# Kernel optimization log

Hardware: AMD Instinct MI355X
Metric: run time of the kernel (lower is better)

## Reference

```python
import jax, jax.numpy as jnp
import numpy as np

N = 20000; E = 320000; IN = 512; H = 4; C = 128; HC = H * C; SD = 2; SE = 128
NEG = 0.01      # nn.LeakyReLU default slope (post-norm activations)
ATT_NEG = 0.2   # GATv2 attention LeakyReLU slope


def _gatv2(x, wl, bl, wr, br, att, bias, src, dst, concat):
    # PyG GATv2Conv (eval mode, add_self_loops already applied to src/dst)
    n = x.shape[0]
    xl = (x @ wl.T + bl).reshape(n, H, C)   # source-side projection
    xr = (x @ wr.T + br).reshape(n, H, C)   # target-side projection
    e = jax.nn.leaky_relu(xl[src] + xr[dst], ATT_NEG)        # [Etot, H, C]
    logits = jnp.einsum('ehc,hc->eh', e, att)                # [Etot, H]
    m = jax.ops.segment_max(logits, dst, num_segments=n)     # segment softmax over dst
    ez = jnp.exp(logits - m[dst])
    denom = jax.ops.segment_sum(ez, dst, num_segments=n)
    alpha = ez / denom[dst]
    out = jax.ops.segment_sum(xl[src] * alpha[:, :, None], dst, num_segments=n)  # [n, H, C]
    out = out.reshape(n, HC) if concat else out.mean(axis=1)
    return out + bias, alpha


def _bn(x, g, b):
    # BatchNorm1d, training-mode batch statistics (biased variance), eps=1e-5
    mu = x.mean(0)
    v = x.var(0)
    return g * (x - mu) * jax.lax.rsqrt(v + 1e-5) + b


def setup_inputs() -> dict:
    key = jax.random.key(0)
    ks = jax.random.split(key, 20)
    p = lambda i, shape: jax.random.normal(ks[i], shape, jnp.float32) * 0.05
    return dict(
        x=jax.random.normal(ks[0], (N, IN), jnp.float32),
        edge_index=jax.random.randint(ks[1], (2, E), 0, N),
        spatial_coords=jax.random.uniform(ks[2], (N, SD), dtype=jnp.float32),
        w1_l=p(3, (HC, IN)), b1_l=jnp.zeros((HC,)), w1_r=p(4, (HC, IN)), b1_r=jnp.zeros((HC,)),
        att1=p(5, (H, C)), bias1=jnp.zeros((HC,)), bn1_g=jnp.ones((HC,)), bn1_b=jnp.zeros((HC,)),
        w2_l=p(6, (HC, HC)), b2_l=jnp.zeros((HC,)), w2_r=p(7, (HC, HC)), b2_r=jnp.zeros((HC,)),
        att2=p(8, (H, C)), bias2=jnp.zeros((HC,)), bn2_g=jnp.ones((HC,)), bn2_b=jnp.zeros((HC,)),
        w3_l=p(9, (HC, HC)), b3_l=jnp.zeros((HC,)), w3_r=p(10, (HC, HC)), b3_r=jnp.zeros((HC,)),
        att3=p(11, (H, C)), bias3=jnp.zeros((C,)), bn3_g=jnp.ones((C,)), bn3_b=jnp.zeros((C,)),
        sp_w1=p(12, (SE, SD)), sp_b1=jnp.zeros((SE,)),
        sp_w2=p(13, (C, SE)), sp_b2=jnp.zeros((C,)),
        mha_in_w=p(14, (3 * SE, SE)), mha_in_b=jnp.zeros((3 * SE,)),
        mha_out_w=p(15, (SE, SE)), mha_out_b=jnp.zeros((SE,)),
        gate_w=p(16, (1, 2 * C)), gate_b=jnp.zeros((1,)),
    )


def reference(x, edge_index, spatial_coords,
              w1_l, b1_l, w1_r, b1_r, att1, bias1, bn1_g, bn1_b,
              w2_l, b2_l, w2_r, b2_r, att2, bias2, bn2_g, bn2_b,
              w3_l, b3_l, w3_r, b3_r, att3, bias3, bn3_g, bn3_b,
              sp_w1, sp_b1, sp_w2, sp_b2,
              mha_in_w, mha_in_b, mha_out_w, mha_out_b,
              gate_w, gate_b):
    loop = jnp.arange(N)
    src = jnp.concatenate([edge_index[0], loop])  # add self loops (PyG default)
    dst = jnp.concatenate([edge_index[1], loop])

    h1, a1 = _gatv2(x, w1_l, b1_l, w1_r, b1_r, att1, bias1, src, dst, True)
    h1 = jax.nn.leaky_relu(_bn(h1, bn1_g, bn1_b), NEG)
    h2, a2 = _gatv2(h1, w2_l, b2_l, w2_r, b2_r, att2, bias2, src, dst, True)
    h2 = jax.nn.leaky_relu(_bn(h2, bn2_g, bn2_b), NEG)
    z, a3 = _gatv2(h2, w3_l, b3_l, w3_r, b3_r, att3, bias3, src, dst, False)
    z = jax.nn.leaky_relu(_bn(z, bn3_g, bn3_b), NEG)

    # spatial embedding MLP (Linear -> LeakyReLU -> Linear -> LeakyReLU)
    emb = jax.nn.leaky_relu(spatial_coords @ sp_w1.T + sp_b1, NEG)
    emb = jax.nn.leaky_relu(emb @ sp_w2.T + sp_b2, NEG)
    # MultiheadAttention over a length-1 sequence: softmax over a single key is 1,
    # so output = W_o (W_v e + b_v) + b_o
    wv = mha_in_w[2 * SE:]
    bv = mha_in_b[2 * SE:]
    sp = (emb @ wv.T + bv) @ mha_out_w.T + mha_out_b  # [N, C]

    gate = jax.nn.softmax(jnp.concatenate([z, sp], axis=-1) @ gate_w.T + gate_b, axis=-1)  # [N,1] (all ones: size-1 softmax, faithful to source)
    z = gate * z + (1.0 - gate) * sp
    return z, a1, a2, a3, gate
```

## Files before the change

### kernel.cpp

```cpp
#include <hip/hip_runtime.h>
#include <math.h>

#define NN 20000
#define EE 320000
#define ETOT 340000
#define MPAD 20096
#define DEGCAP 256

typedef __attribute__((ext_vector_type(8))) short short8;
typedef __attribute__((ext_vector_type(4))) float f32x4;

__device__ __forceinline__ float lrelu(float x, float s) { return fmaxf(x, s * x); }
__device__ __forceinline__ float bf2f(ushort u) {
    union { uint i; float f; } c;
    c.i = ((uint)u) << 16;
    return c.f;
}
__device__ __forceinline__ ushort f2bf(float f) {
    uint u = __float_as_uint(f);
    uint r = (u + 0x7FFFu + ((u >> 16) & 1u)) >> 16;
    return (ushort)r;
}
__device__ __forceinline__ void gload16(const ushort* g, ushort* l) {
    __builtin_amdgcn_global_load_lds((const __attribute__((address_space(1))) void*)g,
                                     (__attribute__((address_space(3))) void*)l, 16, 0, 0);
}

__global__ void k_count(const int* __restrict__ ei, int* __restrict__ counts) {
    int i = blockIdx.x * blockDim.x + threadIdx.x;
    if (i >= ETOT) return;
    int d = (i < EE) ? ei[EE + i] : (i - EE);
    atomicAdd(&counts[d], 1);
}

__global__ __launch_bounds__(1024) void k_scan(const int* __restrict__ counts, int* __restrict__ rstart) {
    __shared__ int sm[1024];
    int t = threadIdx.x;
    const int CH = 20;
    int base = t * CH;
    int loc[CH];
    int s = 0;
#pragma unroll
    for (int j = 0; j < CH; ++j) {
        int idx = base + j;
        int v = (idx < NN) ? counts[idx] : 0;
        loc[j] = s;
        s += v;
    }
    sm[t] = s;
    __syncthreads();
    for (int o = 1; o < 1024; o <<= 1) {
        int v = (t >= o) ? sm[t - o] : 0;
        __syncthreads();
        if (t >= o) sm[t] += v;
        __syncthreads();
    }
    int off = sm[t] - s;
#pragma unroll
    for (int j = 0; j < CH; ++j) {
        int idx = base + j;
        if (idx < NN) rstart[idx] = off + loc[j];
    }
    if (t == 1023) rstart[NN] = sm[1023];
}

__global__ void k_scatter(const int* __restrict__ ei, const int* __restrict__ rstart,
                          int* __restrict__ cursor, int* __restrict__ csr) {
    int i = blockIdx.x * blockDim.x + threadIdx.x;
    if (i >= ETOT) return;
    int d = (i < EE) ? ei[EE + i] : (i - EE);
    int pos = atomicAdd(&cursor[d], 1);
    csr[rstart[d] + pos] = i;
}

__global__ void k_cast(const float* __restrict__ in, ushort* __restrict__ out, int n) {
    int i = (blockIdx.x * blockDim.x + threadIdx.x) * 4;
    if (i >= n) return;
    float4 v = *(const float4*)(in + i);
    uint2 pk;
    pk.x = (uint)f2bf(v.x) | ((uint)f2bf(v.y) << 16);
    pk.y = (uint)f2bf(v.z) | ((uint)f2bf(v.w) << 16);
    *(uint2*)(out + i) = pk;
}

__global__ void k_castw(const float* __restrict__ w0, const float* __restrict__ w1, const float* __restrict__ w2,
                        const float* __restrict__ w3, const float* __restrict__ w4, const float* __restrict__ w5,
                        ushort* __restrict__ out) {
    int i = blockIdx.x * blockDim.x + threadIdx.x;
    if (i >= 6 * 65536) return;
    int which = i >> 16;
    int off = (i & 65535) << 2;
    const float* src = which == 0 ? w0 : which == 1 ? w1 : which == 2 ? w2 : which == 3 ? w3 : which == 4 ? w4 : w5;
    float4 v = *(const float4*)(src + off);
    uint2 pk;
    pk.x = (uint)f2bf(v.x) | ((uint)f2bf(v.y) << 16);
    pk.y = (uint)f2bf(v.z) | ((uint)f2bf(v.w) << 16);
    *(uint2*)(out + which * 262144 + off) = pk;
}

__global__ __launch_bounds__(256) void k_gemm(const ushort* __restrict__ A, const ushort* __restrict__ W,
                                              const float* __restrict__ bias, ushort* __restrict__ C, int M) {
    __shared__ ushort As[4][128][8];
    __shared__ ushort Bs[4][128][8];
    int tid = threadIdx.x;
    int wid = tid >> 6, lane = tid & 63;
    int wm = wid >> 1, wn = wid & 1;
    int bm = blockIdx.x * 128, bn = blockIdx.y * 128;
    int lrow = lane & 15, lslot = lane >> 4;
    int f0 = tid, f1 = tid + 256;
    int r0 = f0 & 127, ks0 = f0 >> 7;
    int r1 = f1 & 127, ks1 = f1 >> 7;
    const ushort* ga0 = A + (size_t)(bm + r0) * 512 + ks0 * 8;
    const ushort* ga1 = A + (size_t)(bm + r1) * 512 + ks1 * 8;
    const ushort* gb0 = W + (size_t)(bn + r0) * 512 + ks0 * 8;
    const ushort* gb1 = W + (size_t)(bn + r1) * 512 + ks1 * 8;
    ushort* lA = &As[0][0][0];
    ushort* lB = &Bs[0][0][0];
    ushort* lA0 = lA + (size_t)(wid * 64) * 8;
    ushort* lA1 = lA + (size_t)(256 + wid * 64) * 8;
    ushort* lB0 = lB + (size_t)(wid * 64) * 8;
    ushort* lB1 = lB + (size_t)(256 + wid * 64) * 8;
    f32x4 acc[4][4] = {};
    for (int k0 = 0; k0 < 512; k0 += 32) {
        gload16(ga0 + k0, lA0);
        gload16(ga1 + k0, lA1);
        gload16(gb0 + k0, lB0);
        gload16(gb1 + k0, lB1);
        __syncthreads();
        short8 af[4], bfr[4];
#pragma unroll
        for (int i = 0; i < 4; ++i) af[i] = *(const short8*)&As[lslot][wm * 64 + i * 16 + lrow][0];
#pragma unroll
        for (int j = 0; j < 4; ++j) bfr[j] = *(const short8*)&Bs[lslot][wn * 64 + j * 16 + lrow][0];
#pragma unroll
        for (int i = 0; i < 4; ++i)
#pragma unroll
            for (int j = 0; j < 4; ++j)
                acc[i][j] = __builtin_amdgcn_mfma_f32_16x16x32_bf16(af[i], bfr[j], acc[i][j], 0, 0, 0);
        __syncthreads();
    }
#pragma unroll
    for (int i = 0; i < 4; ++i) {
#pragma unroll
        for (int j = 0; j < 4; ++j) {
            int gcol = bn + wn * 64 + j * 16 + lrow;
            float bv = bias[gcol];
            int growb = bm + wm * 64 + i * 16 + lslot * 4;
#pragma unroll
            for (int reg = 0; reg < 4; ++reg) {
                int grow = growb + reg;
                if (grow < M) C[(size_t)grow * 512 + gcol] = f2bf(acc[i][j][reg] + bv);
            }
        }
    }
}

__global__ __launch_bounds__(256) void k_fused(const ushort* __restrict__ xl, const ushort* __restrict__ xr,
                                               const float* __restrict__ att, const int* __restrict__ ei,
                                               const int* __restrict__ rstart, const int* __restrict__ csr,
                                               const float* __restrict__ bias, float* __restrict__ alpha,
                                               float* __restrict__ dest, int meanHeads) {
    __shared__ float slg[4][DEGCAP][4];
    __shared__ int ssrc[4][DEGCAP];
    int w = threadIdx.x >> 6, lane = threadIdx.x & 63;
    int node = blockIdx.x * 4 + w;
    int s0 = rstart[node];
    int deg = rstart[node + 1] - s0;
    int hh = lane >> 4;
    short8 xrv = *(const short8*)(xr + (size_t)node * 512 + lane * 8);
    const float4* at = (const float4*)att + lane * 2;
    float4 a0 = at[0], a1 = at[1];
    float attv[8] = {a0.x, a0.y, a0.z, a0.w, a1.x, a1.y, a1.z, a1.w};
    float xrf[8];
#pragma unroll
    for (int j = 0; j < 8; ++j) xrf[j] = bf2f((ushort)xrv[j]);
    for (int i = lane; i < deg; i += 64) {
        int e = csr[s0 + i];
        ssrc[w][i < DEGCAP ? i : 0] = (e < EE) ? ei[e] : e - EE;
    }
    float m = -1e30f, denom = 0.f;
    float acc[8] = {};
    int scur = ssrc[w][0];
    short8 row = *(const short8*)(xl + (size_t)scur * 512 + lane * 8);
    for (int i = 0; i < deg; ++i) {
        short8 rown = row;
        if (i + 1 < deg) {
            int sn = ssrc[w][(i + 1) < DEGCAP ? (i + 1) : 0];
            rown = *(const short8*)(xl + (size_t)sn * 512 + lane * 8);
        }
        float rf[8];
#pragma unroll
        for (int j = 0; j < 8; ++j) rf[j] = bf2f((ushort)row[j]);
        float p = 0.f;
#pragma unroll
        for (int j = 0; j < 8; ++j) {
            float e = rf[j] + xrf[j];
            p = fmaf(fmaxf(e, 0.2f * e), attv[j], p);
        }
        p += __shfl_xor(p, 1);
        p += __shfl_xor(p, 2);
        p += __shfl_xor(p, 4);
        p += __shfl_xor(p, 8);
        if ((lane & 15) == 0 && i < DEGCAP) slg[w][i][hh] = p;
        float mn = fmaxf(m, p);
        float sc = __expf(m - mn);
        float wg = __expf(p - mn);
        denom = denom * sc + wg;
#pragma unroll
        for (int j = 0; j < 8; ++j) acc[j] = acc[j] * sc + wg * rf[j];
        m = mn;
        row = rown;
    }
    float rd = 1.f / denom;
    float m0 = __shfl(m, 0), m1 = __shfl(m, 16), m2 = __shfl(m, 32), m3 = __shfl(m, 48);
    float r0 = __shfl(rd, 0), r1 = __shfl(rd, 16), r2 = __shfl(rd, 32), r3 = __shfl(rd, 48);
    int nal = deg < DEGCAP ? deg : DEGCAP;
    for (int i = lane; i < nal; i += 64) {
        int e = csr[s0 + i];
        float4 l = *(const float4*)&slg[w][i][0];
        float4 av;
        av.x = __expf(l.x - m0) * r0;
        av.y = __expf(l.y - m1) * r1;
        av.z = __expf(l.z - m2) * r2;
        av.w = __expf(l.w - m3) * r3;
        *(float4*)(alpha + (size_t)e * 4) = av;
    }
#pragma unroll
    for (int j = 0; j < 8; ++j) acc[j] *= rd;
    if (!meanHeads) {
        int c = lane * 8;
        float4 o0, o1;
        o0.x = acc[0] + bias[c + 0]; o0.y = acc[1] + bias[c + 1];
        o0.z = acc[2] + bias[c + 2]; o0.w = acc[3] + bias[c + 3];
        o1.x = acc[4] + bias[c + 4]; o1.y = acc[5] + bias[c + 5];
        o1.z = acc[6] + bias[c + 6]; o1.w = acc[7] + bias[c + 7];
        float4* o = (float4*)(dest + (size_t)node * 512 + c);
        o[0] = o0;
        o[1] = o1;
    } else {
#pragma unroll
        for (int j = 0; j < 8; ++j) {
            acc[j] += __shfl_xor(acc[j], 16);
            acc[j] += __shfl_xor(acc[j], 32);
        }
        if (lane < 16) {
            int c = lane * 8;
#pragma unroll
            for (int j = 0; j < 8; ++j) dest[(size_t)node * 128 + c + j] = 0.25f * acc[j] + bias[c + j];
        }
    }
}

__global__ void k_bnstats(const float* __restrict__ X, float* __restrict__ s, float* __restrict__ s2, int ncols) {
    int col = threadIdx.x;
    float a = 0.f, q = 0.f;
    for (int r = blockIdx.x; r < NN; r += gridDim.x) {
        float v = X[(size_t)r * ncols + col];
        a += v;
        q += v * v;
    }
    atomicAdd(&s[col], a);
    atomicAdd(&s2[col], q);
}

__global__ void k_bnfin(const float* __restrict__ s, const float* __restrict__ s2, float* __restrict__ mu,
                        float* __restrict__ rs, int ncols) {
    int c = threadIdx.x;
    if (c < ncols) {
        float m = s[c] * (1.f / NN);
        float v = s2[c] * (1.f / NN) - m * m;
        mu[c] = m;
        rs[c] = rsqrtf(v + 1e-5f);
    }
}

__global__ void k_bnapply(const float* __restrict__ X, const float* __restrict__ g, const float* __restrict__ b,
                          const float* __restrict__ mu, const float* __restrict__ rs, float* __restrict__ Yf,
                          ushort* __restrict__ Yb, int mask4, int n4) {
    int i = blockIdx.x * blockDim.x + threadIdx.x;
    if (i >= n4) return;
    int c = (i & mask4) << 2;
    float4 x = ((const float4*)X)[i];
    float4 G = *(const float4*)(g + c);
    float4 B = *(const float4*)(b + c);
    float4 M = *(const float4*)(mu + c);
    float4 R = *(const float4*)(rs + c);
    float4 y;
    y.x = lrelu(G.x * (x.x - M.x) * R.x + B.x, 0.01f);
    y.y = lrelu(G.y * (x.y - M.y) * R.y + B.y, 0.01f);
    y.z = lrelu(G.z * (x.z - M.z) * R.z + B.z, 0.01f);
    y.w = lrelu(G.w * (x.w - M.w) * R.w + B.w, 0.01f);
    if (Yb) {
        uint2 pk;
        pk.x = (uint)f2bf(y.x) | ((uint)f2bf(y.y) << 16);
        pk.y = (uint)f2bf(y.z) | ((uint)f2bf(y.w) << 16);
        *(uint2*)(Yb + (size_t)i * 4) = pk;
    } else {
        ((float4*)Yf)[i] = y;
    }
}

__global__ void k_gate(float* __restrict__ g) {
    int i = blockIdx.x * blockDim.x + threadIdx.x;
    if (i < NN) g[i] = 1.0f;
}

extern "C" void kernel_launch(void* const* d_in, const int* in_sizes, int n_in,
                              void* d_out, int out_size, void* d_ws, size_t ws_size,
                              hipStream_t stream) {
    const float* x = (const float*)d_in[0];
    const int* ei = (const int*)d_in[1];
    const float* wl[3] = {(const float*)d_in[3], (const float*)d_in[11], (const float*)d_in[19]};
    const float* bl[3] = {(const float*)d_in[4], (const float*)d_in[12], (const float*)d_in[20]};
    const float* wr[3] = {(const float*)d_in[5], (const float*)d_in[13], (const float*)d_in[21]};
    const float* br[3] = {(const float*)d_in[6], (const float*)d_in[14], (const float*)d_in[22]};
    const float* att[3] = {(const float*)d_in[7], (const float*)d_in[15], (const float*)d_in[23]};
    const float* bias[3] = {(const float*)d_in[8], (const float*)d_in[16], (const float*)d_in[24]};
    const float* bng[3] = {(const float*)d_in[9], (const float*)d_in[17], (const float*)d_in[25]};
    const float* bnb[3] = {(const float*)d_in[10], (const float*)d_in[18], (const float*)d_in[26]};

    ushort* a_bf = (ushort*)d_ws;
    ushort* xl_bf = a_bf + (size_t)MPAD * 512;
    ushort* xr_bf = xl_bf + 10240000;
    ushort* wbuf = xr_bf + 10240000;
    float* fp = (float*)(wbuf + 6 * 262144);
    float* h = fp;
    float* zp = h + 10240000;
    float* bsum = zp + 2560000;
    float* bsq = bsum + 512;
    float* bmu = bsq + 512;
    float* brs = bmu + 512;
    int* counts = (int*)(brs + 512);
    int* cursor = counts + NN;
    int* rstart = cursor + NN;
    int* csr = rstart + (NN + 1);
    size_t need = (size_t)((char*)(csr + ETOT) - (char*)d_ws);
    if (ws_size < need) return;

    float* out = (float*)d_out;
    float* zout = out;
    float* aout[3] = {out + 2560000, out + 3920000, out + 5280000};
    float* gout = out + 6640000;

    hipMemsetAsync(counts, 0, 2 * NN * sizeof(int), stream);
    k_count<<<(ETOT + 255) / 256, 256, 0, stream>>>(ei, counts);
    k_scan<<<1, 1024, 0, stream>>>(counts, rstart);
    k_scatter<<<(ETOT + 255) / 256, 256, 0, stream>>>(ei, rstart, cursor, csr);

    hipMemsetAsync(a_bf + (size_t)NN * 512, 0, (size_t)(MPAD - NN) * 512 * sizeof(ushort), stream);
    k_cast<<<(NN * 512 / 4 + 255) / 256, 256, 0, stream>>>(x, a_bf, NN * 512);
    k_castw<<<(6 * 65536 + 255) / 256, 256, 0, stream>>>(wl[0], wr[0], wl[1], wr[1], wl[2], wr[2], wbuf);

    for (int l = 0; l < 3; ++l) {
        const ushort* wlb = wbuf + (size_t)(2 * l) * 262144;
        const ushort* wrb = wbuf + (size_t)(2 * l + 1) * 262144;
        dim3 gg(MPAD / 128, 4);
        k_gemm<<<gg, 256, 0, stream>>>(a_bf, wlb, bl[l], xl_bf, NN);
        k_gemm<<<gg, 256, 0, stream>>>(a_bf, wrb, br[l], xr_bf, NN);
        int ncols = (l == 2) ? 128 : 512;
        float* dest = (l == 2) ? zp : h;
        k_fused<<<NN / 4, 256, 0, stream>>>(xl_bf, xr_bf, att[l], ei, rstart, csr, bias[l], aout[l], dest,
                                            (l == 2) ? 1 : 0);
        hipMemsetAsync(bsum, 0, 1024 * sizeof(float), stream);
        k_bnstats<<<240, ncols, 0, stream>>>(dest, bsum, bsq, ncols);
        k_bnfin<<<1, ncols, 0, stream>>>(bsum, bsq, bmu, brs, ncols);
        int n4 = NN * ncols / 4;
        if (l < 2) {
            k_bnapply<<<(n4 + 255) / 256, 256, 0, stream>>>(dest, bng[l], bnb[l], bmu, brs, nullptr, a_bf,
                                                            ncols / 4 - 1, n4);
        } else {
            k_bnapply<<<(n4 + 255) / 256, 256, 0, stream>>>(dest, bng[l], bnb[l], bmu, brs, zout, nullptr,
                                                            ncols / 4 - 1, n4);
        }
    }
    k_gate<<<(NN + 255) / 256, 256, 0, stream>>>(gout);
}
```

Before: 732.8 us.

## Merge L/R GEMMs, store GAT outputs in bf16, branchy online softmax

Combines the source and target projection GEMMs into one launch with a swizzled tile order and row clamping, removing the padded-row memset. GAT layer outputs are written in bf16, and batchnorm stats/apply read bf16 pairs, cutting intermediate traffic. The online softmax update branches to avoid one exp per edge, and the per-node degree cap in shared memory is halved. This risks precision loss from bf16 intermediates and dropped alphas for nodes with very high degree.

```diff
diff --git a/kernel.cpp b/kernel.cpp
--- a/kernel.cpp
+++ b/kernel.cpp
@@ -4,8 +4,7 @@
 #define NN 20000
 #define EE 320000
 #define ETOT 340000
-#define MPAD 20096
-#define DEGCAP 256
+#define DEGCAP 128
 
 typedef __attribute__((ext_vector_type(8))) short short8;
 typedef __attribute__((ext_vector_type(4))) float f32x4;
@@ -98,20 +97,29 @@
     *(uint2*)(out + which * 262144 + off) = pk;
 }
 
-__global__ __launch_bounds__(256) void k_gemm(const ushort* __restrict__ A, const ushort* __restrict__ W,
-                                              const float* __restrict__ bias, ushort* __restrict__ C, int M) {
+__global__ __launch_bounds__(256) void k_gemm2(const ushort* __restrict__ A, const ushort* __restrict__ W,
+                                               const float* __restrict__ bl, const float* __restrict__ br,
+                                               ushort* __restrict__ XL, ushort* __restrict__ XR) {
     __shared__ ushort As[4][128][8];
     __shared__ ushort Bs[4][128][8];
     int tid = threadIdx.x;
     int wid = tid >> 6, lane = tid & 63;
     int wm = wid >> 1, wn = wid & 1;
-    int bm = blockIdx.x * 128, bn = blockIdx.y * 128;
+    int bid = blockIdx.x;
+    int L = (bid & 7) * 157 + (bid >> 3);
+    int mt = L >> 3, nt = L & 7;
+    int bm = mt * 128, bn = nt * 128;
+    const float* bias = (nt >= 4) ? br : bl;
+    ushort* C = (nt >= 4) ? XR : XL;
+    int cb = bn - ((nt >= 4) ? 512 : 0);
     int lrow = lane & 15, lslot = lane >> 4;
     int f0 = tid, f1 = tid + 256;
     int r0 = f0 & 127, ks0 = f0 >> 7;
     int r1 = f1 & 127, ks1 = f1 >> 7;
-    const ushort* ga0 = A + (size_t)(bm + r0) * 512 + ks0 * 8;
-    const ushort* ga1 = A + (size_t)(bm + r1) * 512 + ks1 * 8;
+    int ar0 = bm + r0; if (ar0 >= NN) ar0 = NN - 1;
+    int ar1 = bm + r1; if (ar1 >= NN) ar1 = NN - 1;
+    const ushort* ga0 = A + (size_t)ar0 * 512 + ks0 * 8;
+    const ushort* ga1 = A + (size_t)ar1 * 512 + ks1 * 8;
     const ushort* gb0 = W + (size_t)(bn + r0) * 512 + ks0 * 8;
     const ushort* gb1 = W + (size_t)(bn + r1) * 512 + ks1 * 8;
     ushort* lA = &As[0][0][0];
@@ -143,13 +151,13 @@
     for (int i = 0; i < 4; ++i) {
 #pragma unroll
         for (int j = 0; j < 4; ++j) {
-            int gcol = bn + wn * 64 + j * 16 + lrow;
+            int gcol = cb + wn * 64 + j * 16 + lrow;
             float bv = bias[gcol];
             int growb = bm + wm * 64 + i * 16 + lslot * 4;
 #pragma unroll
             for (int reg = 0; reg < 4; ++reg) {
                 int grow = growb + reg;
-                if (grow < M) C[(size_t)grow * 512 + gcol] = f2bf(acc[i][j][reg] + bv);
+                if (grow < NN) C[(size_t)grow * 512 + gcol] = f2bf(acc[i][j][reg] + bv);
             }
         }
     }
@@ -159,7 +167,7 @@
                                                const float* __restrict__ att, const int* __restrict__ ei,
                                                const int* __restrict__ rstart, const int* __restrict__ csr,
                                                const float* __restrict__ bias, float* __restrict__ alpha,
-                                               float* __restrict__ dest, int meanHeads) {
+                                               ushort* __restrict__ dest, int meanHeads) {
     __shared__ float slg[4][DEGCAP][4];
     __shared__ int ssrc[4][DEGCAP];
     int w = threadIdx.x >> 6, lane = threadIdx.x & 63;
@@ -202,13 +210,18 @@
         p += __shfl_xor(p, 4);
         p += __shfl_xor(p, 8);
         if ((lane & 15) == 0 && i < DEGCAP) slg[w][i][hh] = p;
-        float mn = fmaxf(m, p);
-        float sc = __expf(m - mn);
-        float wg = __expf(p - mn);
-        denom = denom * sc + wg;
-#pragma unroll
-        for (int j = 0; j < 8; ++j) acc[j] = acc[j] * sc + wg * rf[j];
-        m = mn;
+        if (p <= m) {
+            float wg = __expf(p - m);
+            denom += wg;
+#pragma unroll
+            for (int j = 0; j < 8; ++j) acc[j] = fmaf(wg, rf[j], acc[j]);
+        } else {
+            float sc = __expf(m - p);
+            denom = fmaf(denom, sc, 1.f);
+#pragma unroll
+            for (int j = 0; j < 8; ++j) acc[j] = fmaf(acc[j], sc, rf[j]);
+            m = p;
+        }
         row = rown;
     }
     float rd = 1.f / denom;
@@ -229,14 +242,10 @@
     for (int j = 0; j < 8; ++j) acc[j] *= rd;
     if (!meanHeads) {
         int c = lane * 8;
-        float4 o0, o1;
-        o0.x = acc[0] + bias[c + 0]; o0.y = acc[1] + bias[c + 1];
-        o0.z = acc[2] + bias[c + 2]; o0.w = acc[3] + bias[c + 3];
-        o1.x = acc[4] + bias[c + 4]; o1.y = acc[5] + bias[c + 5];
-        o1.z = acc[6] + bias[c + 6]; o1.w = acc[7] + bias[c + 7];
-        float4* o = (float4*)(dest + (size_t)node * 512 + c);
-        o[0] = o0;
-        o[1] = o1;
+        short8 o;
+#pragma unroll
+        for (int j = 0; j < 8; ++j) o[j] = (short)f2bf(acc[j] + bias[c + j]);
+        *(short8*)(dest + (size_t)node * 512 + c) = o;
     } else {
 #pragma unroll
         for (int j = 0; j < 8; ++j) {
@@ -245,22 +254,29 @@
         }
         if (lane < 16) {
             int c = lane * 8;
-#pragma unroll
-            for (int j = 0; j < 8; ++j) dest[(size_t)node * 128 + c + j] = 0.25f * acc[j] + bias[c + j];
-        }
-    }
-}
-
-__global__ void k_bnstats(const float* __restrict__ X, float* __restrict__ s, float* __restrict__ s2, int ncols) {
-    int col = threadIdx.x;
-    float a = 0.f, q = 0.f;
+            short8 o;
+#pragma unroll
+            for (int j = 0; j < 8; ++j) o[j] = (short)f2bf(0.25f * acc[j] + bias[c + j]);
+            *(short8*)(dest + (size_t)node * 128 + c) = o;
+        }
+    }
+}
+
+__global__ void k_bnstats(const ushort* __restrict__ X, float* __restrict__ s, float* __restrict__ s2, int npairs) {
+    int t = threadIdx.x;
+    if (t >= npairs) return;
+    float a0 = 0.f, a1 = 0.f, q0 = 0.f, q1 = 0.f;
     for (int r = blockIdx.x; r < NN; r += gridDim.x) {
-        float v = X[(size_t)r * ncols + col];
-        a += v;
-        q += v * v;
-    }
-    atomicAdd(&s[col], a);
-    atomicAdd(&s2[col], q);
+        uint p = ((const uint*)X)[r * npairs + t];
+        float v0 = bf2f((ushort)(p & 0xffffu));
+        float v1 = bf2f((ushort)(p >> 16));
+        a0 += v0; q0 += v0 * v0;
+        a1 += v1; q1 += v1 * v1;
+    }
+    atomicAdd(&s[2 * t], a0);
+    atomicAdd(&s[2 * t + 1], a1);
+    atomicAdd(&s2[2 * t], q0);
+    atomicAdd(&s2[2 * t + 1], q1);
 }
 
 __global__ void k_bnfin(const float* __restrict__ s, const float* __restrict__ s2, float* __restrict__ mu,
@@ -274,22 +290,24 @@
     }
 }
 
-__global__ void k_bnapply(const float* __restrict__ X, const float* __restrict__ g, const float* __restrict__ b,
+__global__ void k_bnapply(const ushort* __restrict__ X, const float* __restrict__ g, const float* __restrict__ b,
                           const float* __restrict__ mu, const float* __restrict__ rs, float* __restrict__ Yf,
                           ushort* __restrict__ Yb, int mask4, int n4) {
     int i = blockIdx.x * blockDim.x + threadIdx.x;
     if (i >= n4) return;
     int c = (i & mask4) << 2;
-    float4 x = ((const float4*)X)[i];
+    uint2 p = ((const uint2*)X)[i];
+    float x0 = bf2f((ushort)(p.x & 0xffffu)), x1 = bf2f((ushort)(p.x >> 16));
+    float x2 = bf2f((ushort)(p.y & 0xffffu)), x3 = bf2f((ushort)(p.y >> 16));
     float4 G = *(const float4*)(g + c);
     float4 B = *(const float4*)(b + c);
     float4 M = *(const float4*)(mu + c);
     float4 R = *(const float4*)(rs + c);
     float4 y;
-    y.x = lrelu(G.x * (x.x - M.x) * R.x + B.x, 0.01f);
-    y.y = lrelu(G.y * (x.y - M.y) * R.y + B.y, 0.01f);
-    y.z = lrelu(G.z * (x.z - M.z) * R.z + B.z, 0.01f);
-    y.w = lrelu(G.w * (x.w - M.w) * R.w + B.w, 0.01f);
+    y.x = lrelu(G.x * (x0 - M.x) * R.x + B.x, 0.01f);
+    y.y = lrelu(G.y * (x1 - M.y) * R.y + B.y, 0.01f);
+    y.z = lrelu(G.z * (x2 - M.z) * R.z + B.z, 0.01f);
+    y.w = lrelu(G.w * (x3 - M.w) * R.w + B.w, 0.01f);
     if (Yb) {
         uint2 pk;
         pk.x = (uint)f2bf(y.x) | ((uint)f2bf(y.y) << 16);
@@ -320,13 +338,12 @@
     const float* bnb[3] = {(const float*)d_in[10], (const float*)d_in[18], (const float*)d_in[26]};
 
     ushort* a_bf = (ushort*)d_ws;
-    ushort* xl_bf = a_bf + (size_t)MPAD * 512;
-    ushort* xr_bf = xl_bf + 10240000;
-    ushort* wbuf = xr_bf + 10240000;
+    ushort* xl_bf = a_bf + (size_t)NN * 512;
+    ushort* xr_bf = xl_bf + (size_t)NN * 512;
+    ushort* h_bf = xr_bf + (size_t)NN * 512;
+    ushort* wbuf = h_bf + (size_t)NN * 512;
     float* fp = (float*)(wbuf + 6 * 262144);
-    float* h = fp;
-    float* zp = h + 10240000;
-    float* bsum = zp + 2560000;
+    float* bsum = fp;
     float* bsq = bsum + 512;
     float* bmu = bsq + 512;
     float* brs = bmu + 512;
@@ -347,29 +364,24 @@
     k_scan<<<1, 1024, 0, stream>>>(counts, rstart);
     k_scatter<<<(ETOT + 255) / 256, 256, 0, stream>>>(ei, rstart, cursor, csr);
 
-    hipMemsetAsync(a_bf + (size_t)NN * 512, 0, (size_t)(MPAD - NN) * 512 * sizeof(ushort), stream);
     k_cast<<<(NN * 512 / 4 + 255) / 256, 256, 0, stream>>>(x, a_bf, NN * 512);
     k_castw<<<(6 * 65536 + 255) / 256, 256, 0, stream>>>(wl[0], wr[0], wl[1], wr[1], wl[2], wr[2], wbuf);
 
     for (int l = 0; l < 3; ++l) {
-        const ushort* wlb = wbuf + (size_t)(2 * l) * 262144;
-        const ushort* wrb = wbuf + (size_t)(2 * l + 1) * 262144;
-        dim3 gg(MPAD / 128, 4);
-        k_gemm<<<gg, 256, 0, stream>>>(a_bf, wlb, bl[l], xl_bf, NN);
-        k_gemm<<<gg, 256, 0, stream>>>(a_bf, wrb, br[l], xr_bf, NN);
+        const ushort* wb = wbuf + (size_t)l * 524288;
+        k_gemm2<<<1256, 256, 0, stream>>>(a_bf, wb, bl[l], br[l], xl_bf, xr_bf);
         int ncols = (l == 2) ? 128 : 512;
-        float* dest = (l == 2) ? zp : h;
-        k_fused<<<NN / 4, 256, 0, stream>>>(xl_bf, xr_bf, att[l], ei, rstart, csr, bias[l], aout[l], dest,
+        k_fused<<<NN / 4, 256, 0, stream>>>(xl_bf, xr_bf, att[l], ei, rstart, csr, bias[l], aout[l], h_bf,
                                             (l == 2) ? 1 : 0);
         hipMemsetAsync(bsum, 0, 1024 * sizeof(float), stream);
-        k_bnstats<<<240, ncols, 0, stream>>>(dest, bsum, bsq, ncols);
+        k_bnstats<<<240, 256, 0, stream>>>(h_bf, bsum, bsq, ncols / 2);
         k_bnfin<<<1, ncols, 0, stream>>>(bsum, bsq, bmu, brs, ncols);
         int n4 = NN * ncols / 4;
         if (l < 2) {
-            k_bnapply<<<(n4 + 255) / 256, 256, 0, stream>>>(dest, bng[l], bnb[l], bmu, brs, nullptr, a_bf,
+            k_bnapply<<<(n4 + 255) / 256, 256, 0, stream>>>(h_bf, bng[l], bnb[l], bmu, brs, nullptr, a_bf,
                                                             ncols / 4 - 1, n4);
         } else {
-            k_bnapply<<<(n4 + 255) / 256, 256, 0, stream>>>(dest, bng[l], bnb[l], bmu, brs, zout, nullptr,
+            k_bnapply<<<(n4 + 255) / 256, 256, 0, stream>>>(h_bf, bng[l], bnb[l], bmu, brs, zout, nullptr,
                                                             ncols / 4 - 1, n4);
         }
     }
```

Result: faster. 677.3 us (-7.6%).
